# Kernel optimization log

Measured on AMD Instinct MI355X. Metric: run time of the kernel, lower is better.

## Reference

```python
import jax, jax.numpy as jnp
import numpy as np

B, IN_DIM, OUT_DIM, NNZ = 4096, 9000, 2048, 200000


def setup_inputs() -> dict:
    key = jax.random.key(0)
    k_x, k_r, k_c, k_w, k_b = jax.random.split(key, 5)
    x = jax.random.normal(k_x, (B, IN_DIM), dtype=jnp.float32)
    rows = jax.random.randint(k_r, (NNZ,), 0, IN_DIM, dtype=jnp.int64)
    cols = jax.random.randint(k_c, (NNZ,), 0, OUT_DIM, dtype=jnp.int64)
    nonzero_indices = jnp.stack([rows, cols], axis=1)  # [NNZ, 2]
    weights = jax.random.normal(k_w, (NNZ,), dtype=jnp.float32)
    bias = jax.random.normal(k_b, (OUT_DIM,), dtype=jnp.float32) * 0.1
    return {"x": x, "nonzero_indices": nonzero_indices, "weights": weights, "bias": bias}


def reference(x, nonzero_indices, weights, bias):
    # scatter_nd: build dense [IN_DIM, OUT_DIM] weight matrix from sparse entries
    # (additive semantics, matching tf/torch scatter_nd for duplicate indices)
    W = jnp.zeros((IN_DIM, OUT_DIM), dtype=weights.dtype)
    W = W.at[nonzero_indices[:, 0], nonzero_indices[:, 1]].add(weights)
    # dense mm + bias
    return x @ W + bias
```

## Files before the change

### kernel.cpp

```cpp
#include <hip/hip_runtime.h>

#define B_DIM   4096
#define IN_DIM  9000
#define OUT_DIM 2048
#define NNZ     200000

#define BTILE   128
#define B_TILES (B_DIM / BTILE)
#define COLT_N  64
#define CPB     (OUT_DIM / COLT_N)
#define THREADS 1024
#define CAP     160

typedef float v2f __attribute__((ext_vector_type(2)));

#define FB_BTILE  8
#define FB_SEGLEN 1360
#define FB_NSEG   7
#define FB_NKEY   (FB_NSEG * OUT_DIM)
#define FB_XPAD   12


__global__ void scatter_direct_kernel(const int* __restrict__ idx,
                                      const float* __restrict__ w,
                                      int* __restrict__ cur,
                                      uint2* __restrict__ entries) {
    int i = blockIdx.x * blockDim.x + threadIdx.x;
    if (i >= NNZ) return;
    int r = idx[2 * i];
    int c = idx[2 * i + 1];
    if ((unsigned)r < IN_DIM && (unsigned)c < OUT_DIM) {
        int slot = atomicAdd(&cur[c], 1);
        if (slot < CAP)
            entries[c * CAP + slot] =
                make_uint2((unsigned)r * (B_DIM / 2), __float_as_uint(w[i]));
    }
}

__global__ __launch_bounds__(256) void transpose_kernel(const float* __restrict__ x,
                                                        unsigned int* __restrict__ xTu,
                                                        int* __restrict__ cur) {
    __shared__ float tile[64][65];
    int r0 = blockIdx.x * 64;
    int b0 = blockIdx.y * 64;
    int t = threadIdx.x;

    if (blockIdx.x == 0 && blockIdx.y == 0) {
        for (int i = t; i < OUT_DIM; i += 256) cur[i] = 0;
    }

    if (r0 + 64 <= IN_DIM) {
        int j4 = (t & 15) * 4;
        int i0 = t >> 4;
#pragma unroll
        for (int p = 0; p < 4; ++p) {
            int i = i0 + 16 * p;
            float4 v = *(const float4*)&x[(size_t)(b0 + i) * IN_DIM + r0 + j4];
            tile[i][j4 + 0] = v.x;
            tile[i][j4 + 1] = v.y;
            tile[i][j4 + 2] = v.z;
            tile[i][j4 + 3] = v.w;
        }
    } else {
        int i0 = t >> 6, j = t & 63;
        int r = r0 + j;
#pragma unroll
        for (int ii = 0; ii < 16; ++ii) {
            int i = i0 + 4 * ii;
            tile[i][j] = (r < IN_DIM) ? x[(size_t)(b0 + i) * IN_DIM + r] : 0.f;
        }
    }
    __syncthreads();
    {
        int m  = t & 31;
        int j0 = t >> 5;
#pragma unroll
        for (int p = 0; p < 8; ++p) {
            int jr = j0 + 8 * p;
            int r = r0 + jr;
            if (r < IN_DIM) {
                unsigned int a = __float_as_uint(tile[2 * m][jr]);
                unsigned int b = __float_as_uint(tile[2 * m + 1][jr]);
                unsigned int ha = (a + 0x7fffu + ((a >> 16) & 1u)) >> 16;
                unsigned int hb = (b + 0x7fffu + ((b >> 16) & 1u)) & 0xffff0000u;
                xTu[(size_t)r * (B_DIM / 2) + (b0 >> 1) + m] = ha | hb;
            }
        }
    }
}

#define F8PK(E, U)                                                        \
    { _Pragma("unroll")                                                   \
      for (int k = 0; k < 8; ++k) {                                       \
          v2f w2 = __uint_as_float(E[k].y);                               \
          v2f u2;                                                         \
          u2.x = __uint_as_float(U[k] << 16);                             \
          u2.y = __uint_as_float(U[k] & 0xffff0000u);                     \
          A[k] = __builtin_elementwise_fma(w2, u2, A[k]);                 \
      } }

__global__ __launch_bounds__(THREADS, 8) void spmm_xt_kernel(
    const unsigned int* __restrict__ xTu,
    const float*        __restrict__ bias,
    const int*          __restrict__ cnt,
    const uint2*        __restrict__ entries,
    float* __restrict__ out) {

    __shared__ float oacc[CPB * BTILE];
    __shared__ int ctr;

    const int t = threadIdx.x;
    const int lane = t & 63;

    if (t == 0) ctr = 0;
    __syncthreads();

    const int bid = blockIdx.x;
    const int xcd    = bid & 7;
    const int colT   = (bid >> 3) & 63;
    const int group  = bid >> 9;
    const int b_tile = group * 8 + xcd;

    const int laneoff = b_tile * (BTILE / 2) + lane;

    for (;;) {
        int colv = 0;
        if (lane == 0) colv = atomicAdd(&ctr, 1);
        colv = __shfl(colv, 0);
        if (colv >= CPB) break;
        const int col = __builtin_amdgcn_readfirstlane(colv);
        const int c = colT * CPB + col;
        const int s = c * CAP;
        int n = __builtin_amdgcn_readfirstlane(cnt[c]);
        n = (n > CAP) ? CAP : n;
        const int e = s + n;

        v2f A[8];
#pragma unroll
        for (int k = 0; k < 8; ++k) A[k] = (v2f)0.f;

        int jj = s;
        const int nfull = n >> 3;

        if (nfull >= 2) {
            uint2 Ea[8], Eb[8];
            unsigned int ua[8];
#pragma unroll
            for (int k = 0; k < 8; ++k) Ea[k] = entries[jj + k];
#pragma unroll
            for (int k = 0; k < 8; ++k) Eb[k] = entries[jj + 8 + k];
#pragma unroll
            for (int k = 0; k < 8; ++k) ua[k] = xTu[Ea[k].x + laneoff];

            for (int ib = 0; ib < nfull - 2; ++ib) {
                uint2 Ec[8];
#pragma unroll
                for (int k = 0; k < 8; ++k) Ec[k] = entries[jj + 16 + k];
                unsigned int ub[8];
#pragma unroll
                for (int k = 0; k < 8; ++k) ub[k] = xTu[Eb[k].x + laneoff];
                F8PK(Ea, ua);
#pragma unroll
                for (int k = 0; k < 8; ++k) { Ea[k] = Eb[k]; Eb[k] = Ec[k]; ua[k] = ub[k]; }
                jj += 8;
            }
            {
                unsigned int ub[8];
#pragma unroll
                for (int k = 0; k < 8; ++k) ub[k] = xTu[Eb[k].x + laneoff];
                F8PK(Ea, ua);
                F8PK(Eb, ub);
                jj += 16;
            }
        } else if (nfull == 1) {
            uint2 Ea[8];
            unsigned int ua[8];
#pragma unroll
            for (int k = 0; k < 8; ++k) Ea[k] = entries[jj + k];
#pragma unroll
            for (int k = 0; k < 8; ++k) ua[k] = xTu[Ea[k].x + laneoff];
            F8PK(Ea, ua);
            jj += 8;
        }
        for (; jj < e; ++jj) {
            uint2 E0 = entries[jj];
            unsigned int u0 = xTu[E0.x + laneoff];
            v2f w2 = __uint_as_float(E0.y);
            v2f u2;
            u2.x = __uint_as_float(u0 << 16);
            u2.y = __uint_as_float(u0 & 0xffff0000u);
            A[0] = __builtin_elementwise_fma(w2, u2, A[0]);
        }

        v2f S = ((A[0] + A[1]) + (A[2] + A[3])) + ((A[4] + A[5]) + (A[6] + A[7]));

        const int bl0 = 2 * lane;
        oacc[col * BTILE + (bl0 ^ (col & 31))]       = S.x;
        oacc[col * BTILE + ((bl0 + 1) ^ (col & 31))] = S.y;
    }
    __syncthreads();

    const int tc = t & 31;
    const int tb = t >> 5;
    const int C0 = colT * CPB;
    const size_t B0 = (size_t)b_tile * BTILE;
    const float bi = bias[C0 + tc];
#pragma unroll
    for (int bl = 0; bl < BTILE / 32; ++bl) {
        int b = tb + 32 * bl;
        out[(B0 + b) * OUT_DIM + C0 + tc] = oacc[tc * BTILE + (b ^ (tc & 31))] + bi;
    }
}


__global__ void fb_hist_kernel(const int* __restrict__ idx, int* __restrict__ cnt) {
    int i = blockIdx.x * blockDim.x + threadIdx.x;
    if (i >= NNZ) return;
    int r = idx[2 * i];
    int c = idx[2 * i + 1];
    if ((unsigned)r < IN_DIM && (unsigned)c < OUT_DIM) {
        int seg = r / FB_SEGLEN;
        atomicAdd(&cnt[seg * OUT_DIM + c], 1);
    }
}

__global__ __launch_bounds__(1024) void fb_scan_kernel(const int* __restrict__ cnt,
                                                       int* __restrict__ key_start) {
    __shared__ int lds_c[FB_NKEY];
    __shared__ int lds_p[1024];
    int t = threadIdx.x;
    for (int i = t; i < FB_NKEY; i += 1024) lds_c[i] = cnt[i];
    __syncthreads();
    const int CH = FB_NKEY / 1024;
    int base = t * CH;
    int partial = 0;
    for (int i = 0; i < CH; ++i) partial += lds_c[base + i];
    lds_p[t] = partial;
    __syncthreads();
    for (int off = 1; off < 1024; off <<= 1) {
        int v = (t >= off) ? lds_p[t - off] : 0;
        __syncthreads();
        lds_p[t] += v;
        __syncthreads();
    }
    int run = (t == 0) ? 0 : lds_p[t - 1];
    for (int i = 0; i < CH; ++i) { key_start[base + i] = run; run += lds_c[base + i]; }
    if (t == 1023) key_start[FB_NKEY] = lds_p[1023];
}

__global__ void fb_scatter_kernel(const int* __restrict__ idx,
                                  const float* __restrict__ w,
                                  const int* __restrict__ key_start,
                                  int* __restrict__ cur,
                                  uint2* __restrict__ entries) {
    int i = blockIdx.x * blockDim.x + threadIdx.x;
    if (i >= NNZ) return;
    int r = idx[2 * i];
    int c = idx[2 * i + 1];
    if ((unsigned)r < IN_DIM && (unsigned)c < OUT_DIM) {
        int seg = r / FB_SEGLEN;
        int key = seg * OUT_DIM + c;
        int pos = key_start[key] + atomicAdd(&cur[key], 1);
        entries[pos] = make_uint2((unsigned)(r - seg * FB_SEGLEN), __float_as_uint(w[i]));
    }
}

__global__ __launch_bounds__(1024, 8) void fb_spmm_kernel(
    const float* __restrict__ x,
    const float* __restrict__ bias,
    const int*   __restrict__ key_start,
    const uint2* __restrict__ entries,
    float* __restrict__ out) {

    __shared__ float xs[FB_SEGLEN * FB_XPAD];
    const int t = threadIdx.x;
    const size_t b0 = (size_t)blockIdx.x * FB_BTILE;
    const int c0 = t;
    const int c1 = t + 1024;

    float acc0[FB_BTILE], acc1[FB_BTILE];
#pragma unroll
    for (int b = 0; b < FB_BTILE; ++b) { acc0[b] = 0.f; acc1[b] = 0.f; }

    for (int seg = 0; seg < FB_NSEG; ++seg) {
        const int rbase = seg * FB_SEGLEN;
        const int rlen = (IN_DIM - rbase < FB_SEGLEN) ? (IN_DIM - rbase) : FB_SEGLEN;
        __syncthreads();
#pragma unroll
        for (int b = 0; b < FB_BTILE; ++b) {
            const float* __restrict__ src = x + (b0 + b) * IN_DIM + rbase;
            for (int r = t; r < rlen; r += 1024) xs[r * FB_XPAD + b] = src[r];
        }
        __syncthreads();
        for (int cc = 0; cc < 2; ++cc) {
            int c = cc ? c1 : c0;
            float* acc = cc ? acc1 : acc0;
            int s = key_start[seg * OUT_DIM + c];
            int e = key_start[seg * OUT_DIM + c + 1];
            for (int j = s; j < e; ++j) {
                uint2 en = entries[j];
                float wv = __uint_as_float(en.y);
                const float4* xr = (const float4*)(xs + en.x * FB_XPAD);
                float4 lo = xr[0];
                float4 hi = xr[1];
                acc[0] = fmaf(wv, lo.x, acc[0]);
                acc[1] = fmaf(wv, lo.y, acc[1]);
                acc[2] = fmaf(wv, lo.z, acc[2]);
                acc[3] = fmaf(wv, lo.w, acc[3]);
                acc[4] = fmaf(wv, hi.x, acc[4]);
                acc[5] = fmaf(wv, hi.y, acc[5]);
                acc[6] = fmaf(wv, hi.z, acc[6]);
                acc[7] = fmaf(wv, hi.w, acc[7]);
            }
        }
    }
    const float bi0 = bias[c0];
    const float bi1 = bias[c1];
#pragma unroll
    for (int b = 0; b < FB_BTILE; ++b) {
        out[(b0 + b) * OUT_DIM + c0] = acc0[b] + bi0;
        out[(b0 + b) * OUT_DIM + c1] = acc1[b] + bi1;
    }
}


extern "C" void kernel_launch(void* const* d_in, const int* in_sizes, int n_in,
                              void* d_out, int out_size, void* d_ws, size_t ws_size,
                              hipStream_t stream) {
    const float* x    = (const float*)d_in[0];
    const int*   idx  = (const int*)  d_in[1];
    const float* w    = (const float*)d_in[2];
    const float* bias = (const float*)d_in[3];
    float* out = (float*)d_out;

    const size_t xT_bytes  = (size_t)IN_DIM * B_DIM * 2;
    const size_t int_bytes = ((size_t)2048 * 4 + 15) & ~(size_t)15;
    const size_t need = xT_bytes + int_bytes + (size_t)OUT_DIM * CAP * 8;

    if (ws_size >= need) {
        unsigned int* xTu = (unsigned int*)d_ws;
        int* cur       = (int*)((char*)d_ws + xT_bytes);
        uint2* entries = (uint2*)((char*)d_ws + xT_bytes + int_bytes);

        dim3 tg((IN_DIM + 63) / 64, B_DIM / 64);
        transpose_kernel<<<tg, 256, 0, stream>>>(x, xTu, cur);
        scatter_direct_kernel<<<(NNZ + 255) / 256, 256, 0, stream>>>(idx, w, cur, entries);
        spmm_xt_kernel<<<B_TILES * COLT_N, THREADS, 0, stream>>>(
            xTu, bias, cur, entries, out);
    } else {
        int* cnt       = (int*)d_ws;
        int* cur       = cnt + FB_NKEY;
        int* key_start = cur + FB_NKEY;
        size_t ent_off = ((size_t)(3 * FB_NKEY + 1) * sizeof(int) + 15) & ~(size_t)15;
        uint2* entries = (uint2*)((char*)d_ws + ent_off);

        hipMemsetAsync(cnt, 0, 2 * FB_NKEY * sizeof(int), stream);
        fb_hist_kernel<<<(NNZ + 255) / 256, 256, 0, stream>>>(idx, cnt);
        fb_scan_kernel<<<1, 1024, 0, stream>>>(cnt, key_start);
        fb_scatter_kernel<<<(NNZ + 255) / 256, 256, 0, stream>>>(idx, w, key_start, cur, entries);
        fb_spmm_kernel<<<B_DIM / FB_BTILE, 1024, 0, stream>>>(x, bias, key_start, entries, out);
    }
}
```

Measured before the change: 176.9 us.

## Widen batch tile to 256 with 8-byte bf16x4 gathers per lane

The batch tile doubles, and each lane now gathers a uint2 holding four bf16 batch values per sparse entry, feeding two packed-FMA accumulator sets. Each sparse entry's index and weight are now loaded once per 256 batch rows instead of 128, which halves entry-list traffic and per-entry loop overhead, and the gathers become wider. In exchange the kernel launches half as many blocks, uses more registers per lane and needs a larger LDS output tile with an adjusted swizzle, so occupancy and load balance may suffer.

```diff
diff --git a/kernel.cpp b/kernel.cpp
--- a/kernel.cpp
+++ b/kernel.cpp
@@ -5,7 +5,7 @@
 #define OUT_DIM 2048
 #define NNZ     200000
 
-#define BTILE   128
+#define BTILE   256
 #define B_TILES (B_DIM / BTILE)
 #define COLT_N  64
 #define CPB     (OUT_DIM / COLT_N)
@@ -33,7 +33,7 @@
         int slot = atomicAdd(&cur[c], 1);
         if (slot < CAP)
             entries[c * CAP + slot] =
-                make_uint2((unsigned)r * (B_DIM / 2), __float_as_uint(w[i]));
+                make_uint2((unsigned)r * (B_DIM / 4), __float_as_uint(w[i]));
     }
 }
 
@@ -89,21 +89,24 @@
     }
 }
 
-#define F8PK(E, U)                                                        \
+#define F8PK2(E, U)                                                       \
     { _Pragma("unroll")                                                   \
       for (int k = 0; k < 8; ++k) {                                       \
           v2f w2 = __uint_as_float(E[k].y);                               \
-          v2f u2;                                                         \
-          u2.x = __uint_as_float(U[k] << 16);                             \
-          u2.y = __uint_as_float(U[k] & 0xffff0000u);                     \
-          A[k] = __builtin_elementwise_fma(w2, u2, A[k]);                 \
+          v2f ux, uy;                                                     \
+          ux.x = __uint_as_float(U[k].x << 16);                           \
+          ux.y = __uint_as_float(U[k].x & 0xffff0000u);                   \
+          uy.x = __uint_as_float(U[k].y << 16);                           \
+          uy.y = __uint_as_float(U[k].y & 0xffff0000u);                   \
+          A[k & 3] = __builtin_elementwise_fma(w2, ux, A[k & 3]);         \
+          B[k & 3] = __builtin_elementwise_fma(w2, uy, B[k & 3]);         \
       } }
 
 __global__ __launch_bounds__(THREADS, 8) void spmm_xt_kernel(
-    const unsigned int* __restrict__ xTu,
-    const float*        __restrict__ bias,
-    const int*          __restrict__ cnt,
-    const uint2*        __restrict__ entries,
+    const uint2* __restrict__ xTu2,
+    const float* __restrict__ bias,
+    const int*   __restrict__ cnt,
+    const uint2* __restrict__ entries,
     float* __restrict__ out) {
 
     __shared__ float oacc[CPB * BTILE];
@@ -121,7 +124,7 @@
     const int group  = bid >> 9;
     const int b_tile = group * 8 + xcd;
 
-    const int laneoff = b_tile * (BTILE / 2) + lane;
+    const int laneoff = b_tile * (BTILE / 4) + lane;
 
     for (;;) {
         int colv = 0;
@@ -135,68 +138,75 @@
         n = (n > CAP) ? CAP : n;
         const int e = s + n;
 
-        v2f A[8];
-#pragma unroll
-        for (int k = 0; k < 8; ++k) A[k] = (v2f)0.f;
+        v2f A[4], B[4];
+#pragma unroll
+        for (int k = 0; k < 4; ++k) { A[k] = (v2f)0.f; B[k] = (v2f)0.f; }
 
         int jj = s;
         const int nfull = n >> 3;
 
         if (nfull >= 2) {
             uint2 Ea[8], Eb[8];
-            unsigned int ua[8];
+            uint2 ua[8];
 #pragma unroll
             for (int k = 0; k < 8; ++k) Ea[k] = entries[jj + k];
 #pragma unroll
             for (int k = 0; k < 8; ++k) Eb[k] = entries[jj + 8 + k];
 #pragma unroll
-            for (int k = 0; k < 8; ++k) ua[k] = xTu[Ea[k].x + laneoff];
+            for (int k = 0; k < 8; ++k) ua[k] = xTu2[Ea[k].x + laneoff];
 
             for (int ib = 0; ib < nfull - 2; ++ib) {
                 uint2 Ec[8];
 #pragma unroll
                 for (int k = 0; k < 8; ++k) Ec[k] = entries[jj + 16 + k];
-                unsigned int ub[8];
-#pragma unroll
-                for (int k = 0; k < 8; ++k) ub[k] = xTu[Eb[k].x + laneoff];
-                F8PK(Ea, ua);
+                uint2 ub[8];
+#pragma unroll
+                for (int k = 0; k < 8; ++k) ub[k] = xTu2[Eb[k].x + laneoff];
+                F8PK2(Ea, ua);
 #pragma unroll
                 for (int k = 0; k < 8; ++k) { Ea[k] = Eb[k]; Eb[k] = Ec[k]; ua[k] = ub[k]; }
                 jj += 8;
             }
             {
-                unsigned int ub[8];
-#pragma unroll
-                for (int k = 0; k < 8; ++k) ub[k] = xTu[Eb[k].x + laneoff];
-                F8PK(Ea, ua);
-                F8PK(Eb, ub);
+                uint2 ub[8];
+#pragma unroll
+                for (int k = 0; k < 8; ++k) ub[k] = xTu2[Eb[k].x + laneoff];
+                F8PK2(Ea, ua);
+                F8PK2(Eb, ub);
                 jj += 16;
             }
         } else if (nfull == 1) {
             uint2 Ea[8];
-            unsigned int ua[8];
+            uint2 ua[8];
 #pragma unroll
             for (int k = 0; k < 8; ++k) Ea[k] = entries[jj + k];
 #pragma unroll
-            for (int k = 0; k < 8; ++k) ua[k] = xTu[Ea[k].x + laneoff];
-            F8PK(Ea, ua);
+            for (int k = 0; k < 8; ++k) ua[k] = xTu2[Ea[k].x + laneoff];
+            F8PK2(Ea, ua);
             jj += 8;
         }
         for (; jj < e; ++jj) {
             uint2 E0 = entries[jj];
-            unsigned int u0 = xTu[E0.x + laneoff];
+            uint2 u0 = xTu2[E0.x + laneoff];
             v2f w2 = __uint_as_float(E0.y);
-            v2f u2;
-            u2.x = __uint_as_float(u0 << 16);
-            u2.y = __uint_as_float(u0 & 0xffff0000u);
-            A[0] = __builtin_elementwise_fma(w2, u2, A[0]);
-        }
-
-        v2f S = ((A[0] + A[1]) + (A[2] + A[3])) + ((A[4] + A[5]) + (A[6] + A[7]));
-
-        const int bl0 = 2 * lane;
-        oacc[col * BTILE + (bl0 ^ (col & 31))]       = S.x;
-        oacc[col * BTILE + ((bl0 + 1) ^ (col & 31))] = S.y;
+            v2f ux, uy;
+            ux.x = __uint_as_float(u0.x << 16);
+            ux.y = __uint_as_float(u0.x & 0xffff0000u);
+            uy.x = __uint_as_float(u0.y << 16);
+            uy.y = __uint_as_float(u0.y & 0xffff0000u);
+            A[0] = __builtin_elementwise_fma(w2, ux, A[0]);
+            B[0] = __builtin_elementwise_fma(w2, uy, B[0]);
+        }
+
+        v2f S0 = (A[0] + A[1]) + (A[2] + A[3]);
+        v2f S1 = (B[0] + B[1]) + (B[2] + B[3]);
+
+        const int swz = (col & 31) << 2;
+        const int b0 = 4 * lane;
+        oacc[col * BTILE + ((b0 + 0) ^ swz)] = S0.x;
+        oacc[col * BTILE + ((b0 + 1) ^ swz)] = S0.y;
+        oacc[col * BTILE + ((b0 + 2) ^ swz)] = S1.x;
+        oacc[col * BTILE + ((b0 + 3) ^ swz)] = S1.y;
     }
     __syncthreads();
 
@@ -205,10 +215,11 @@
     const int C0 = colT * CPB;
     const size_t B0 = (size_t)b_tile * BTILE;
     const float bi = bias[C0 + tc];
+    const int swz = (tc & 31) << 2;
 #pragma unroll
     for (int bl = 0; bl < BTILE / 32; ++bl) {
         int b = tb + 32 * bl;
-        out[(B0 + b) * OUT_DIM + C0 + tc] = oacc[tc * BTILE + (b ^ (tc & 31))] + bi;
+        out[(B0 + b) * OUT_DIM + C0 + tc] = oacc[tc * BTILE + (b ^ swz)] + bi;
     }
 }
 
@@ -346,7 +357,7 @@
         transpose_kernel<<<tg, 256, 0, stream>>>(x, xTu, cur);
         scatter_direct_kernel<<<(NNZ + 255) / 256, 256, 0, stream>>>(idx, w, cur, entries);
         spmm_xt_kernel<<<B_TILES * COLT_N, THREADS, 0, stream>>>(
-            xTu, bias, cur, entries, out);
+            (const uint2*)xTu, bias, cur, entries, out);
     } else {
         int* cnt       = (int*)d_ws;
         int* cur       = cnt + FB_NKEY;
```

Result: slower. 184.0 us (+4.0%).
